# Kernel tuning notes

Measured on AMD Instinct MI355X. Metric: run time of the kernel, lower is better.

The kernel has to match this reference:

```python
import jax, jax.numpy as jnp
import numpy as np

N = 100000
E = 1600000
IN_DIM = 128
HID = 128
OUT_DIM = 64
ORDER = 4


def setup_inputs() -> dict:
    key = jax.random.key(0)
    ks = jax.random.split(key, 10)
    x = jax.random.normal(ks[0], (N, IN_DIM), dtype=jnp.float32)
    edge_index = jax.random.randint(ks[1], (2, E), 0, N, dtype=jnp.int64)
    gen_edge_index = jax.random.randint(ks[2], (2, E), 0, N, dtype=jnp.int64)
    s = 1.0 / np.sqrt(IN_DIM)
    w_orig = jax.random.normal(ks[3], (ORDER + 1, IN_DIM, HID), dtype=jnp.float32) * s
    b_orig = jax.random.normal(ks[4], (ORDER + 1, HID), dtype=jnp.float32) * s
    w_aug = jax.random.normal(ks[5], (ORDER + 1, IN_DIM, HID), dtype=jnp.float32) * s
    b_aug = jax.random.normal(ks[6], (ORDER + 1, HID), dtype=jnp.float32) * s
    fusion_weight = jnp.ones((2,), dtype=jnp.float32)
    clf_w = jax.random.normal(ks[7], (HID, OUT_DIM), dtype=jnp.float32) / np.sqrt(HID)
    clf_b = jax.random.normal(ks[8], (OUT_DIM,), dtype=jnp.float32) / np.sqrt(HID)
    return {"x": x, "edge_index": edge_index, "gen_edge_index": gen_edge_index,
            "w_orig": w_orig, "b_orig": b_orig, "w_aug": w_aug, "b_aug": b_aug,
            "fusion_weight": fusion_weight, "clf_w": clf_w, "clf_b": clf_b}


def _beta_wavelet(x, edge_index, W, b, num_nodes):
    # add self loops
    loop = jnp.arange(num_nodes, dtype=edge_index.dtype)
    row = jnp.concatenate([edge_index[0], loop])
    col = jnp.concatenate([edge_index[1], loop])
    # symmetric normalization D^{-1/2} A D^{-1/2}
    deg = jax.ops.segment_sum(jnp.ones_like(col, dtype=x.dtype), col, num_segments=num_nodes)
    dinv = jnp.where(deg > 0, deg ** -0.5, 0.0)
    norm = dinv[row] * dinv[col]  # [E+N]
    out = x @ W[0] + b[0]
    Tx = x
    for i in range(1, ORDER + 1):
        msg = norm[:, None] * Tx[row]                      # gather + scale [E+N, D]
        Tx = jax.ops.segment_sum(msg, col, num_segments=num_nodes)  # scatter_add
        out = out + Tx @ W[i] + b[i]
    return jax.nn.relu(out)


def reference(x, edge_index, gen_edge_index, w_orig, b_orig, w_aug, b_aug, fusion_weight, clf_w, clf_b):
    num_nodes = x.shape[0]
    h_orig = _beta_wavelet(x, edge_index, w_orig, b_orig, num_nodes)
    h_aug = _beta_wavelet(x, gen_edge_index, w_aug, b_aug, num_nodes)
    w = jax.nn.softmax(fusion_weight)
    h_final = w[0] * h_orig + w[1] * h_aug
    return h_final @ clf_w + clf_b
```

## Files before the change

kernel.cpp:

```cpp
#include <hip/hip_runtime.h>

#define N_NODES 100000
#define NPAD    100096
#define NE      1600000
#define DIM     128
#define ODIM    64
#define NORDER  4
#define KTOT    640
#define NB      391

typedef _Float16 h8 __attribute__((ext_vector_type(8)));
typedef float f4 __attribute__((ext_vector_type(4)));

__device__ __forceinline__ float2 up2(unsigned p) {
    union { unsigned u; _Float16 h[2]; } c; c.u = p;
    return make_float2((float)c.h[0], (float)c.h[1]);
}
__device__ __forceinline__ unsigned pk2(float x, float y) {
    union { unsigned u; _Float16 h[2]; } c;
    c.h[0] = (_Float16)x; c.h[1] = (_Float16)y;
    return c.u;
}
__device__ __forceinline__ unsigned short f2hbits(float x) {
    union { _Float16 h; unsigned short s; } c;
    c.h = (_Float16)x;
    return c.s;
}
__device__ __forceinline__ void async_cp16(const void* g, void* l) {
    __builtin_amdgcn_global_load_lds((const __attribute__((address_space(1))) void*)g,
                                     (__attribute__((address_space(3))) void*)l, 16, 0, 0);
}

__global__ __launch_bounds__(256) void zero_b(int* __restrict__ bhist) {
    int i = blockIdx.x * 256 + threadIdx.x;
    if (i < NB) bhist[i] = 0;
}

__global__ __launch_bounds__(256) void hist_edges(const int* __restrict__ colp,
                                                  int* __restrict__ bhist) {
    __shared__ int lh[NB];
    int t = threadIdx.x;
    for (int i = t; i < NB; i += 256) lh[i] = 0;
    __syncthreads();
    int base = blockIdx.x * 2048 + t;
#pragma unroll
    for (int j = 0; j < 8; ++j) {
        int e = base + j * 256;
        if (e < NE) atomicAdd(&lh[colp[e] >> 8], 1);
    }
    __syncthreads();
    for (int i = t; i < NB; i += 256) if (lh[i]) atomicAdd(&bhist[i], lh[i]);
}

__global__ void bscan(const int* __restrict__ bhist,
                      int* __restrict__ boff,
                      int* __restrict__ bcursor) {
    if (threadIdx.x == 0 && blockIdx.x == 0) {
        int run = 0;
        for (int i = 0; i < NB; ++i) {
            boff[i] = run; bcursor[i] = run; run += bhist[i];
        }
        boff[NB] = run;
    }
}

__global__ __launch_bounds__(256) void part_edges(const int* __restrict__ rowp,
                                                  const int* __restrict__ colp,
                                                  int* __restrict__ bcursor,
                                                  int2* __restrict__ pairs) {
    __shared__ int lh[NB];
    __shared__ int lpos[NB];
    int t = threadIdx.x;
    for (int i = t; i < NB; i += 256) lh[i] = 0;
    __syncthreads();
    int base = blockIdx.x * 4096 + t;
    int rank[16];
    short bk[16];
#pragma unroll
    for (int j = 0; j < 16; ++j) {
        int e = base + j * 256;
        rank[j] = -1;
        if (e < NE) {
            int b = colp[e] >> 8;
            bk[j] = (short)b;
            rank[j] = atomicAdd(&lh[b], 1);
        }
    }
    __syncthreads();
    for (int i = t; i < NB; i += 256) {
        int n = lh[i];
        lpos[i] = n ? atomicAdd(&bcursor[i], n) : 0;
    }
    __syncthreads();
#pragma unroll
    for (int j = 0; j < 16; ++j) {
        int e = base + j * 256;
        if (e < NE) {
            int b = bk[j];
            pairs[lpos[b] + rank[j]] = make_int2(rowp[e], colp[e]);
        }
    }
}

__global__ __launch_bounds__(256) void count_fine(const int2* __restrict__ pairs,
                                                  const int* __restrict__ boff,
                                                  int* __restrict__ cnt) {
    __shared__ int lcnt[256];
    int t = threadIdx.x, b = blockIdx.x;
    lcnt[t] = 0;
    __syncthreads();
    int s = boff[b], e = boff[b + 1];
    int base = b << 8;
    for (int i = s + t; i < e; i += 256)
        atomicAdd(&lcnt[pairs[i].y - base], 1);
    __syncthreads();
    int node = base + t;
    if (node < N_NODES) cnt[node] = lcnt[t];
}

__global__ __launch_bounds__(256) void scan_block(const int* __restrict__ cnt,
                                                  int* __restrict__ excl,
                                                  int* __restrict__ bsum) {
    __shared__ int lds[256];
    int t = threadIdx.x, b = blockIdx.x;
    int base = b * 1024 + t * 4;
    int v0 = (base + 0 < N_NODES) ? cnt[base + 0] : 0;
    int v1 = (base + 1 < N_NODES) ? cnt[base + 1] : 0;
    int v2 = (base + 2 < N_NODES) ? cnt[base + 2] : 0;
    int v3 = (base + 3 < N_NODES) ? cnt[base + 3] : 0;
    int tot = v0 + v1 + v2 + v3;
    lds[t] = tot;
    __syncthreads();
    for (int off = 1; off < 256; off <<= 1) {
        int x = (t >= off) ? lds[t - off] : 0;
        __syncthreads();
        lds[t] += x;
        __syncthreads();
    }
    int run = lds[t] - tot;
    if (t == 255) bsum[b] = lds[255];
    if (base + 0 < N_NODES) excl[base + 0] = run; run += v0;
    if (base + 1 < N_NODES) excl[base + 1] = run; run += v1;
    if (base + 2 < N_NODES) excl[base + 2] = run; run += v2;
    if (base + 3 < N_NODES) excl[base + 3] = run;
}

__global__ void scan_mid(int* __restrict__ bsum, int nb) {
    if (threadIdx.x == 0 && blockIdx.x == 0) {
        int run = 0;
        for (int i = 0; i < nb; ++i) { int x = bsum[i]; bsum[i] = run; run += x; }
    }
}

__global__ __launch_bounds__(256) void scan_add(int* __restrict__ ptrv,
                                                const int* __restrict__ bsum,
                                                const int* __restrict__ cnt,
                                                float* __restrict__ dinv) {
    int i = blockIdx.x * 256 + threadIdx.x;
    if (i < N_NODES) {
        dinv[i] = rsqrtf((float)(cnt[i] + 1));
        ptrv[i] += bsum[i >> 10];
    }
    if (i == 0) ptrv[N_NODES] = NE;
}

__global__ __launch_bounds__(256) void fine_csr(const int2* __restrict__ pairs,
                                                const int* __restrict__ boff,
                                                const int* __restrict__ ptrv,
                                                int* __restrict__ srcv) {
    __shared__ int lcnt[256];
    int t = threadIdx.x, b = blockIdx.x;
    lcnt[t] = 0;
    __syncthreads();
    int s = boff[b], e = boff[b + 1];
    int base = b << 8;
    for (int i = s + t; i < e; i += 256) {
        int2 pr = pairs[i];
        int pos = ptrv[pr.y] + atomicAdd(&lcnt[pr.y - base], 1);
        srcv[pos] = pr.x;
    }
}

__global__ __launch_bounds__(256) void xcast(const float* __restrict__ x,
                                             unsigned* __restrict__ Tbig) {
    int idx = blockIdx.x * 256 + threadIdx.x;
    if (idx >= NPAD * 64) return;
    int m = idx >> 6, u = idx & 63;
    int e = (m << 7) + u * 2;
    float a = (m < N_NODES) ? x[e]     : 0.f;
    float b = (m < N_NODES) ? x[e + 1] : 0.f;
    Tbig[m * 320 + u] = pk2(a, b);
}

__global__ __launch_bounds__(256) void wcast(const float* __restrict__ Wo,
                                             const float* __restrict__ Wa,
                                             unsigned short* __restrict__ Wt) {
    int idx = blockIdx.x * 256 + threadIdx.x;
    if (idx >= 2 * 5 * DIM * DIM) return;
    int g   = idx / (5 * DIM * DIM);
    int rem = idx % (5 * DIM * DIM);
    int i   = rem / (DIM * DIM);
    int r2  = rem % (DIM * DIM);
    int k8  = r2 >> 10;
    int n   = (r2 >> 3) & 127;
    int k7  = r2 & 7;
    int k   = k8 * 8 + k7;
    const float* W = g ? Wa : Wo;
    Wt[idx] = f2hbits(W[(i * DIM + k) * DIM + n]);
}

__global__ __launch_bounds__(256) void propagate(const unsigned* __restrict__ Tin,
                                                 unsigned* __restrict__ Tout,
                                                 const int* __restrict__ ptrv,
                                                 const int* __restrict__ srcv,
                                                 const float* __restrict__ dinv) {
    int gid  = blockIdx.x * 256 + threadIdx.x;
    int lane = threadIdx.x & 63;
    int v    = __builtin_amdgcn_readfirstlane(gid >> 6);
    if (v >= N_NODES) return;
    float dv = dinv[v];
    float2 self = up2(Tin[v * 320 + lane]);
    float ax = dv * dv * self.x;
    float ay = dv * dv * self.y;
    int beg = ptrv[v], end = ptrv[v + 1];
    int k = beg;
    for (; k + 16 <= end; k += 16) {
        int u[16];
#pragma unroll
        for (int j = 0; j < 16; ++j) u[j] = srcv[k + j];
        float2 tt[16];
#pragma unroll
        for (int j = 0; j < 16; ++j) tt[j] = up2(Tin[u[j] * 320 + lane]);
        float w[16];
#pragma unroll
        for (int j = 0; j < 16; ++j) w[j] = dinv[u[j]] * dv;
#pragma unroll
        for (int j = 0; j < 16; ++j) { ax += w[j] * tt[j].x; ay += w[j] * tt[j].y; }
    }
    for (; k + 4 <= end; k += 4) {
        int u[4];
#pragma unroll
        for (int j = 0; j < 4; ++j) u[j] = srcv[k + j];
        float2 tt[4];
#pragma unroll
        for (int j = 0; j < 4; ++j) tt[j] = up2(Tin[u[j] * 320 + lane]);
        float w[4];
#pragma unroll
        for (int j = 0; j < 4; ++j) w[j] = dinv[u[j]] * dv;
#pragma unroll
        for (int j = 0; j < 4; ++j) { ax += w[j] * tt[j].x; ay += w[j] * tt[j].y; }
    }
    for (; k < end; ++k) {
        int u = srcv[k];
        float w = dinv[u] * dv;
        float2 t = up2(Tin[u * 320 + lane]);
        ax += w * t.x; ay += w * t.y;
    }
    Tout[v * 320 + lane] = pk2(ax, ay);
}

__global__ __launch_bounds__(256, 3) void gemmK(const unsigned short* __restrict__ A,
                                                const unsigned short* __restrict__ Wt,
                                                float* __restrict__ C) {
    __shared__ unsigned short Bl[DIM * DIM];
    int t = threadIdx.x;
    int lane = t & 63, wv = t >> 6;
    int m0 = blockIdx.x * 128 + wv * 32;
    int l15 = lane & 15, q = lane >> 4;
    f4 acc[2][8];
#pragma unroll
    for (int mt = 0; mt < 2; ++mt)
#pragma unroll
        for (int nt = 0; nt < 8; ++nt) acc[mt][nt] = (f4)(0.f);

#pragma unroll
    for (int i = 0; i < 5; ++i) {
        const unsigned short* WtI = Wt + (size_t)i * DIM * DIM;
        h8 af[2][4];
#pragma unroll
        for (int mt = 0; mt < 2; ++mt)
#pragma unroll
            for (int kc = 0; kc < 4; ++kc)
                af[mt][kc] = *(const h8*)(A + (size_t)(m0 + mt * 16 + l15) * KTOT
                                            + i * DIM + (kc * 4 + q) * 8);
#pragma unroll
        for (int c = 0; c < 8; ++c) {
            int ci = c * 4 + wv;
            async_cp16(WtI + ci * 512 + lane * 8, &Bl[ci * 512]);
        }
        __syncthreads();
#pragma unroll
        for (int kc = 0; kc < 4; ++kc) {
            int c = kc * 4 + q;
#pragma unroll
            for (int nt = 0; nt < 8; ++nt) {
                h8 bf = *(const h8*)&Bl[(size_t)(c * 128 + nt * 16 + l15) * 8];
                acc[0][nt] = __builtin_amdgcn_mfma_f32_16x16x32_f16(af[0][kc], bf, acc[0][nt], 0, 0, 0);
                acc[1][nt] = __builtin_amdgcn_mfma_f32_16x16x32_f16(af[1][kc], bf, acc[1][nt], 0, 0, 0);
            }
        }
        __syncthreads();
    }
#pragma unroll
    for (int mt = 0; mt < 2; ++mt)
#pragma unroll
        for (int nt = 0; nt < 8; ++nt)
#pragma unroll
            for (int r = 0; r < 4; ++r)
                C[(size_t)(m0 + mt * 16 + q * 4 + r) * DIM + nt * 16 + l15] = acc[mt][nt][r];
}

__global__ __launch_bounds__(256) void fuse_clf(const float* __restrict__ accO,
                                                const float* __restrict__ accA,
                                                const float* __restrict__ bO,
                                                const float* __restrict__ bA,
                                                const float* __restrict__ fw,
                                                const float* __restrict__ clfW,
                                                const float* __restrict__ clfB,
                                                float* __restrict__ out) {
    __shared__ float Wl[DIM * ODIM];
    __shared__ float Hl[32 * DIM];
    __shared__ float bs[2][DIM];
    int t = threadIdx.x;
    float f0 = fw[0], f1 = fw[1];
    float m = fmaxf(f0, f1);
    float e0 = expf(f0 - m), e1 = expf(f1 - m);
    float sw0 = e0 / (e0 + e1), sw1 = e1 / (e0 + e1);
    if (t < 128) {
        float s = 0.f;
        for (int i = 0; i <= NORDER; ++i) s += bO[i * DIM + t];
        bs[0][t] = s;
    } else {
        int j = t - 128;
        float s = 0.f;
        for (int i = 0; i <= NORDER; ++i) s += bA[i * DIM + j];
        bs[1][j] = s;
    }
    for (int i = 0; i < 8; ++i) {
        int idx = (i * 256 + t) * 4;
        *(float4*)&Wl[idx] = *(const float4*)&clfW[idx];
    }
    __syncthreads();
    int rowBase = blockIdx.x * 32;
    for (int i = 0; i < 4; ++i) {
        int idx = (i * 256 + t) * 4;
        int kcol = idx & 127;
        float4 a = *(const float4*)&accO[rowBase * DIM + idx];
        float4 b = *(const float4*)&accA[rowBase * DIM + idx];
        float4 h;
        h.x = sw0 * fmaxf(a.x + bs[0][kcol + 0], 0.f) + sw1 * fmaxf(b.x + bs[1][kcol + 0], 0.f);
        h.y = sw0 * fmaxf(a.y + bs[0][kcol + 1], 0.f) + sw1 * fmaxf(b.y + bs[1][kcol + 1], 0.f);
        h.z = sw0 * fmaxf(a.z + bs[0][kcol + 2], 0.f) + sw1 * fmaxf(b.z + bs[1][kcol + 2], 0.f);
        h.w = sw0 * fmaxf(a.w + bs[0][kcol + 3], 0.f) + sw1 * fmaxf(b.w + bs[1][kcol + 3], 0.f);
        *(float4*)&Hl[idx] = h;
    }
    __syncthreads();
    int lane = t & 63, w = t >> 6;
    int c2 = (lane & 31) * 2;
    int r0 = w * 8 + (lane >> 5) * 4;
    float acc[4][2];
    for (int j = 0; j < 4; ++j) { acc[j][0] = 0.f; acc[j][1] = 0.f; }
    for (int k0 = 0; k0 < DIM; k0 += 4) {
        float4 a0 = *(const float4*)&Hl[(r0 + 0) * DIM + k0];
        float4 a1 = *(const float4*)&Hl[(r0 + 1) * DIM + k0];
        float4 a2 = *(const float4*)&Hl[(r0 + 2) * DIM + k0];
        float4 a3 = *(const float4*)&Hl[(r0 + 3) * DIM + k0];
#define FSTEP(comp, kk)                                                      \
        {                                                                    \
            float2 wv = *(const float2*)&Wl[(k0 + kk) * ODIM + c2];          \
            acc[0][0] += a0.comp * wv.x; acc[0][1] += a0.comp * wv.y;        \
            acc[1][0] += a1.comp * wv.x; acc[1][1] += a1.comp * wv.y;        \
            acc[2][0] += a2.comp * wv.x; acc[2][1] += a2.comp * wv.y;        \
            acc[3][0] += a3.comp * wv.x; acc[3][1] += a3.comp * wv.y;        \
        }
        FSTEP(x, 0) FSTEP(y, 1) FSTEP(z, 2) FSTEP(w, 3)
#undef FSTEP
    }
    float2 cb2 = *(const float2*)&clfB[c2];
    for (int j = 0; j < 4; ++j) {
        float2 o = make_float2(acc[j][0] + cb2.x, acc[j][1] + cb2.y);
        *(float2*)&out[(rowBase + r0 + j) * ODIM + c2] = o;
    }
}

extern "C" void kernel_launch(void* const* d_in, const int* in_sizes, int n_in,
                              void* d_out, int out_size, void* d_ws, size_t ws_size,
                              hipStream_t stream) {
    const float* x   = (const float*)d_in[0];
    const int*   ei  = (const int*)d_in[1];
    const int*   gi  = (const int*)d_in[2];
    const float* w_o = (const float*)d_in[3];
    const float* b_o = (const float*)d_in[4];
    const float* w_a = (const float*)d_in[5];
    const float* b_a = (const float*)d_in[6];
    const float* fw  = (const float*)d_in[7];
    const float* cw  = (const float*)d_in[8];
    const float* cb  = (const float*)d_in[9];
    float* out = (float*)d_out;

    char* p = (char*)d_ws;
    auto alloc = [&](size_t bytes) {
        void* r = (void*)p;
        p += (bytes + 255) & ~(size_t)255;
        return r;
    };
    unsigned* Tbig = (unsigned*)alloc((size_t)NPAD * 320 * 4);
    float* acc_o = (float*)alloc((size_t)NPAD * DIM * 4);
    float* acc_a = (float*)alloc((size_t)NPAD * DIM * 4);
    unsigned short* Wt = (unsigned short*)alloc((size_t)2 * 5 * DIM * DIM * 2);
    float* dinv  = (float*)alloc((size_t)N_NODES * 4);
    int2* pairs  = (int2*)alloc((size_t)NE * 8);
    int* csr_src = (int*)alloc((size_t)NE * 4);
    int* csr_ptr = (int*)alloc((size_t)(N_NODES + 1) * 4);
    int* cnt     = (int*)alloc((size_t)N_NODES * 4);
    int* bsum    = (int*)alloc(128 * 4);
    int* bhist   = (int*)alloc((size_t)NB * 4);
    int* boff    = (int*)alloc((size_t)(NB + 1) * 4);
    int* bcursor = (int*)alloc((size_t)NB * 4);

    const int gN  = (N_NODES + 255) / 256;
    const int gH2 = (NE + 2047) / 2048;
    const int gH4 = (NE + 4095) / 4096;
    const int gS  = (N_NODES + 1023) / 1024;
    const int gP  = (N_NODES * 64 + 255) / 256;
    const int gX  = (NPAD * 64 + 255) / 256;
    const int gW  = (2 * 5 * DIM * DIM + 255) / 256;
    const int gM  = NPAD / 128;
    const int gF  = N_NODES / 32;

    xcast<<<gX, 256, 0, stream>>>(x, Tbig);
    wcast<<<gW, 256, 0, stream>>>(w_o, w_a, Wt);

    for (int g = 0; g < 2; ++g) {
        const int* edges = g ? gi : ei;
        const int* rowp = edges;
        const int* colp = edges + NE;
        float* acc = g ? acc_a : acc_o;
        const unsigned short* Wtg = Wt + (size_t)g * 5 * DIM * DIM;

        zero_b<<<2, 256, 0, stream>>>(bhist);
        hist_edges<<<gH2, 256, 0, stream>>>(colp, bhist);
        bscan<<<1, 64, 0, stream>>>(bhist, boff, bcursor);
        part_edges<<<gH4, 256, 0, stream>>>(rowp, colp, bcursor, pairs);
        count_fine<<<NB, 256, 0, stream>>>(pairs, boff, cnt);
        scan_block<<<gS, 256, 0, stream>>>(cnt, csr_ptr, bsum);
        scan_mid<<<1, 64, 0, stream>>>(bsum, gS);
        scan_add<<<gN, 256, 0, stream>>>(csr_ptr, bsum, cnt, dinv);
        fine_csr<<<NB, 256, 0, stream>>>(pairs, boff, csr_ptr, csr_src);

        for (int i = 1; i <= NORDER; ++i)
            propagate<<<gP, 256, 0, stream>>>(Tbig + (i - 1) * 64, Tbig + i * 64,
                                              csr_ptr, csr_src, dinv);

        gemmK<<<gM, 256, 0, stream>>>((const unsigned short*)Tbig, Wtg, acc);
    }
    fuse_clf<<<gF, 256, 0, stream>>>(acc_o, acc_a, b_o, b_a, fw, cw, cb, out);
}
```

Before: 937.3 us.

## Batch CSR construction for both graphs and pack edge pairs into 32-bit words

```diff
diff --git a/kernel.cpp b/kernel.cpp
--- a/kernel.cpp
+++ b/kernel.cpp
@@ -31,65 +31,91 @@
                                      (__attribute__((address_space(3))) void*)l, 16, 0, 0);
 }
 
-__global__ __launch_bounds__(256) void zero_b(int* __restrict__ bhist) {
-    int i = blockIdx.x * 256 + threadIdx.x;
-    if (i < NB) bhist[i] = 0;
-}
-
-__global__ __launch_bounds__(256) void hist_edges(const int* __restrict__ colp,
+
+__global__ __launch_bounds__(256) void hist_edges(const int* __restrict__ e0,
+                                                  const int* __restrict__ e1,
                                                   int* __restrict__ bhist) {
     __shared__ int lh[NB];
     int t = threadIdx.x;
+    int g = blockIdx.x >= 782;
+    int blk = g ? (blockIdx.x - 782) : blockIdx.x;
+    const int* colp = (g ? e1 : e0) + NE;
+    int* bh = bhist + g * NB;
     for (int i = t; i < NB; i += 256) lh[i] = 0;
     __syncthreads();
-    int base = blockIdx.x * 2048 + t;
+    int base = blk * 2048 + t;
 #pragma unroll
     for (int j = 0; j < 8; ++j) {
         int e = base + j * 256;
         if (e < NE) atomicAdd(&lh[colp[e] >> 8], 1);
     }
     __syncthreads();
-    for (int i = t; i < NB; i += 256) if (lh[i]) atomicAdd(&bhist[i], lh[i]);
-}
-
-__global__ void bscan(const int* __restrict__ bhist,
-                      int* __restrict__ boff,
-                      int* __restrict__ bcursor) {
-    if (threadIdx.x == 0 && blockIdx.x == 0) {
-        int run = 0;
-        for (int i = 0; i < NB; ++i) {
-            boff[i] = run; bcursor[i] = run; run += bhist[i];
-        }
-        boff[NB] = run;
-    }
-}
-
-__global__ __launch_bounds__(256) void part_edges(const int* __restrict__ rowp,
-                                                  const int* __restrict__ colp,
+    for (int i = t; i < NB; i += 256) if (lh[i]) atomicAdd(&bh[i], lh[i]);
+}
+
+__global__ void wave_scan(const int* __restrict__ in,
+                          int* __restrict__ oexcl,
+                          int* __restrict__ ocur,
+                          int n, int with_cur) {
+    int wv = threadIdx.x >> 6, lane = threadIdx.x & 63;
+    if (wv >= 2) return;
+    const int* I = in + wv * n;
+    int* O = oexcl + wv * (n + 1);
+    int* C = ocur + wv * n;
+    int carry = 0;
+    for (int base = 0; base < n; base += 64) {
+        int i = base + lane;
+        int v = (i < n) ? I[i] : 0;
+        int s = v;
+#pragma unroll
+        for (int off = 1; off < 64; off <<= 1) {
+            int x = __shfl_up(s, off, 64);
+            if (lane >= off) s += x;
+        }
+        int excl = carry + s - v;
+        if (i < n) {
+            O[i] = excl;
+            if (with_cur) C[i] = excl;
+        }
+        carry += __shfl(s, 63, 64);
+    }
+    if (lane == 0) O[n] = carry;
+}
+
+__global__ __launch_bounds__(256) void part_edges(const int* __restrict__ e0,
+                                                  const int* __restrict__ e1,
                                                   int* __restrict__ bcursor,
-                                                  int2* __restrict__ pairs) {
+                                                  unsigned* __restrict__ pairs) {
     __shared__ int lh[NB];
     __shared__ int lpos[NB];
     int t = threadIdx.x;
+    int g = blockIdx.x >= NB;
+    int blk = g ? (blockIdx.x - NB) : blockIdx.x;
+    const int* rowp = (g ? e1 : e0);
+    const int* colp = rowp + NE;
+    int* bc = bcursor + g * NB;
+    unsigned* pr = pairs + (size_t)g * NE;
     for (int i = t; i < NB; i += 256) lh[i] = 0;
     __syncthreads();
-    int base = blockIdx.x * 4096 + t;
+    int base = blk * 4096 + t;
     int rank[16];
     short bk[16];
+    unsigned char lcv[16];
 #pragma unroll
     for (int j = 0; j < 16; ++j) {
         int e = base + j * 256;
         rank[j] = -1;
         if (e < NE) {
-            int b = colp[e] >> 8;
-            bk[j] = (short)b;
-            rank[j] = atomicAdd(&lh[b], 1);
+            int c = colp[e];
+            bk[j] = (short)(c >> 8);
+            lcv[j] = (unsigned char)(c & 255);
+            rank[j] = atomicAdd(&lh[c >> 8], 1);
         }
     }
     __syncthreads();
     for (int i = t; i < NB; i += 256) {
         int n = lh[i];
-        lpos[i] = n ? atomicAdd(&bcursor[i], n) : 0;
+        lpos[i] = n ? atomicAdd(&bc[i], n) : 0;
     }
     __syncthreads();
 #pragma unroll
@@ -97,87 +123,82 @@
         int e = base + j * 256;
         if (e < NE) {
             int b = bk[j];
-            pairs[lpos[b] + rank[j]] = make_int2(rowp[e], colp[e]);
-        }
-    }
-}
-
-__global__ __launch_bounds__(256) void count_fine(const int2* __restrict__ pairs,
-                                                  const int* __restrict__ boff,
-                                                  int* __restrict__ cnt) {
+            pr[lpos[b] + rank[j]] = ((unsigned)rowp[e] << 8) | lcv[j];
+        }
+    }
+}
+
+__global__ __launch_bounds__(256) void cnt_scan(const unsigned* __restrict__ pairs,
+                                                const int* __restrict__ boff,
+                                                int* __restrict__ ptrv,
+                                                float* __restrict__ dinv,
+                                                int* __restrict__ bsum) {
     __shared__ int lcnt[256];
-    int t = threadIdx.x, b = blockIdx.x;
+    __shared__ int lscan[256];
+    int t = threadIdx.x;
+    int g = blockIdx.x >= NB;
+    int b = g ? (blockIdx.x - NB) : blockIdx.x;
+    const unsigned* pr = pairs + (size_t)g * NE;
+    const int* bo = boff + g * (NB + 1);
+    int* pv = ptrv + g * (N_NODES + 1);
+    float* dv = dinv + g * N_NODES;
+    int* bs = bsum + g * NB;
     lcnt[t] = 0;
     __syncthreads();
-    int s = boff[b], e = boff[b + 1];
-    int base = b << 8;
+    int s = bo[b], e = bo[b + 1];
     for (int i = s + t; i < e; i += 256)
-        atomicAdd(&lcnt[pairs[i].y - base], 1);
-    __syncthreads();
-    int node = base + t;
-    if (node < N_NODES) cnt[node] = lcnt[t];
-}
-
-__global__ __launch_bounds__(256) void scan_block(const int* __restrict__ cnt,
-                                                  int* __restrict__ excl,
-                                                  int* __restrict__ bsum) {
-    __shared__ int lds[256];
-    int t = threadIdx.x, b = blockIdx.x;
-    int base = b * 1024 + t * 4;
-    int v0 = (base + 0 < N_NODES) ? cnt[base + 0] : 0;
-    int v1 = (base + 1 < N_NODES) ? cnt[base + 1] : 0;
-    int v2 = (base + 2 < N_NODES) ? cnt[base + 2] : 0;
-    int v3 = (base + 3 < N_NODES) ? cnt[base + 3] : 0;
-    int tot = v0 + v1 + v2 + v3;
-    lds[t] = tot;
+        atomicAdd(&lcnt[pr[i] & 255u], 1);
+    __syncthreads();
+    int v = lcnt[t];
+    lscan[t] = v;
     __syncthreads();
     for (int off = 1; off < 256; off <<= 1) {
-        int x = (t >= off) ? lds[t - off] : 0;
+        int x = (t >= off) ? lscan[t - off] : 0;
         __syncthreads();
-        lds[t] += x;
+        lscan[t] += x;
         __syncthreads();
     }
-    int run = lds[t] - tot;
-    if (t == 255) bsum[b] = lds[255];
-    if (base + 0 < N_NODES) excl[base + 0] = run; run += v0;
-    if (base + 1 < N_NODES) excl[base + 1] = run; run += v1;
-    if (base + 2 < N_NODES) excl[base + 2] = run; run += v2;
-    if (base + 3 < N_NODES) excl[base + 3] = run;
-}
-
-__global__ void scan_mid(int* __restrict__ bsum, int nb) {
-    if (threadIdx.x == 0 && blockIdx.x == 0) {
-        int run = 0;
-        for (int i = 0; i < nb; ++i) { int x = bsum[i]; bsum[i] = run; run += x; }
-    }
-}
-
-__global__ __launch_bounds__(256) void scan_add(int* __restrict__ ptrv,
-                                                const int* __restrict__ bsum,
-                                                const int* __restrict__ cnt,
-                                                float* __restrict__ dinv) {
-    int i = blockIdx.x * 256 + threadIdx.x;
-    if (i < N_NODES) {
-        dinv[i] = rsqrtf((float)(cnt[i] + 1));
-        ptrv[i] += bsum[i >> 10];
-    }
-    if (i == 0) ptrv[N_NODES] = NE;
-}
-
-__global__ __launch_bounds__(256) void fine_csr(const int2* __restrict__ pairs,
+    int node = (b << 8) + t;
+    if (node < N_NODES) {
+        pv[node] = lscan[t] - v;
+        dv[node] = rsqrtf((float)(v + 1));
+    }
+    if (t == 255) bs[b] = lscan[255];
+}
+
+__global__ __launch_bounds__(256) void scan_addk(int* __restrict__ ptrv,
+                                                 const int* __restrict__ bmid) {
+    int t = threadIdx.x;
+    int g = blockIdx.x >= NB;
+    int b = g ? (blockIdx.x - NB) : blockIdx.x;
+    int* pv = ptrv + g * (N_NODES + 1);
+    const int* bm = bmid + g * (NB + 1);
+    int node = (b << 8) + t;
+    if (node < N_NODES) pv[node] += bm[b];
+    if (b == 0 && t == 0) pv[N_NODES] = NE;
+}
+
+__global__ __launch_bounds__(256) void fine_csr(const unsigned* __restrict__ pairs,
                                                 const int* __restrict__ boff,
                                                 const int* __restrict__ ptrv,
                                                 int* __restrict__ srcv) {
     __shared__ int lcnt[256];
-    int t = threadIdx.x, b = blockIdx.x;
+    int t = threadIdx.x;
+    int g = blockIdx.x >= NB;
+    int b = g ? (blockIdx.x - NB) : blockIdx.x;
+    const unsigned* pr = pairs + (size_t)g * NE;
+    const int* bo = boff + g * (NB + 1);
+    const int* pv = ptrv + g * (N_NODES + 1);
+    int* sv = srcv + (size_t)g * NE;
     lcnt[t] = 0;
     __syncthreads();
-    int s = boff[b], e = boff[b + 1];
+    int s = bo[b], e = bo[b + 1];
     int base = b << 8;
     for (int i = s + t; i < e; i += 256) {
-        int2 pr = pairs[i];
-        int pos = ptrv[pr.y] + atomicAdd(&lcnt[pr.y - base], 1);
-        srcv[pos] = pr.x;
+        unsigned pk = pr[i];
+        int lc = (int)(pk & 255u);
+        int pos = pv[base + lc] + atomicAdd(&lcnt[lc], 1);
+        sv[pos] = (int)(pk >> 8);
     }
 }
 
@@ -408,20 +429,16 @@
     float* acc_o = (float*)alloc((size_t)NPAD * DIM * 4);
     float* acc_a = (float*)alloc((size_t)NPAD * DIM * 4);
     unsigned short* Wt = (unsigned short*)alloc((size_t)2 * 5 * DIM * DIM * 2);
-    float* dinv  = (float*)alloc((size_t)N_NODES * 4);
-    int2* pairs  = (int2*)alloc((size_t)NE * 8);
-    int* csr_src = (int*)alloc((size_t)NE * 4);
-    int* csr_ptr = (int*)alloc((size_t)(N_NODES + 1) * 4);
-    int* cnt     = (int*)alloc((size_t)N_NODES * 4);
-    int* bsum    = (int*)alloc(128 * 4);
-    int* bhist   = (int*)alloc((size_t)NB * 4);
-    int* boff    = (int*)alloc((size_t)(NB + 1) * 4);
-    int* bcursor = (int*)alloc((size_t)NB * 4);
-
-    const int gN  = (N_NODES + 255) / 256;
-    const int gH2 = (NE + 2047) / 2048;
-    const int gH4 = (NE + 4095) / 4096;
-    const int gS  = (N_NODES + 1023) / 1024;
+    float* dinv  = (float*)alloc((size_t)2 * N_NODES * 4);
+    unsigned* pairs = (unsigned*)alloc((size_t)2 * NE * 4);
+    int* csr_src = (int*)alloc((size_t)2 * NE * 4);
+    int* csr_ptr = (int*)alloc((size_t)2 * (N_NODES + 1) * 4);
+    int* bhist   = (int*)alloc((size_t)2 * NB * 4);
+    int* boff    = (int*)alloc((size_t)2 * (NB + 1) * 4);
+    int* bcursor = (int*)alloc((size_t)2 * NB * 4);
+    int* bsum    = (int*)alloc((size_t)2 * NB * 4);
+    int* bmid    = (int*)alloc((size_t)2 * (NB + 1) * 4);
+
     const int gP  = (N_NODES * 64 + 255) / 256;
     const int gX  = (NPAD * 64 + 255) / 256;
     const int gW  = (2 * 5 * DIM * DIM + 255) / 256;
@@ -431,26 +448,25 @@
     xcast<<<gX, 256, 0, stream>>>(x, Tbig);
     wcast<<<gW, 256, 0, stream>>>(w_o, w_a, Wt);
 
+    hipMemsetAsync(bhist, 0, (size_t)2 * NB * 4, stream);
+    hist_edges<<<2 * 782, 256, 0, stream>>>(ei, gi, bhist);
+    wave_scan<<<1, 128, 0, stream>>>(bhist, boff, bcursor, NB, 1);
+    part_edges<<<2 * NB, 256, 0, stream>>>(ei, gi, bcursor, pairs);
+    cnt_scan<<<2 * NB, 256, 0, stream>>>(pairs, boff, csr_ptr, dinv, bsum);
+    wave_scan<<<1, 128, 0, stream>>>(bsum, bmid, bcursor, NB, 0);
+    scan_addk<<<2 * NB, 256, 0, stream>>>(csr_ptr, bmid);
+    fine_csr<<<2 * NB, 256, 0, stream>>>(pairs, boff, csr_ptr, csr_src);
+
     for (int g = 0; g < 2; ++g) {
-        const int* edges = g ? gi : ei;
-        const int* rowp = edges;
-        const int* colp = edges + NE;
         float* acc = g ? acc_a : acc_o;
         const unsigned short* Wtg = Wt + (size_t)g * 5 * DIM * DIM;
-
-        zero_b<<<2, 256, 0, stream>>>(bhist);
-        hist_edges<<<gH2, 256, 0, stream>>>(colp, bhist);
-        bscan<<<1, 64, 0, stream>>>(bhist, boff, bcursor);
-        part_edges<<<gH4, 256, 0, stream>>>(rowp, colp, bcursor, pairs);
-        count_fine<<<NB, 256, 0, stream>>>(pairs, boff, cnt);
-        scan_block<<<gS, 256, 0, stream>>>(cnt, csr_ptr, bsum);
-        scan_mid<<<1, 64, 0, stream>>>(bsum, gS);
-        scan_add<<<gN, 256, 0, stream>>>(csr_ptr, bsum, cnt, dinv);
-        fine_csr<<<NB, 256, 0, stream>>>(pairs, boff, csr_ptr, csr_src);
+        const int* pv = csr_ptr + g * (N_NODES + 1);
+        const int* sv = csr_src + (size_t)g * NE;
+        const float* dv = dinv + (size_t)g * N_NODES;
 
         for (int i = 1; i <= NORDER; ++i)
             propagate<<<gP, 256, 0, stream>>>(Tbig + (i - 1) * 64, Tbig + i * 64,
-                                              csr_ptr, csr_src, dinv);
+                                              pv, sv, dv);
 
         gemmK<<<gM, 256, 0, stream>>>((const unsigned short*)Tbig, Wtg, acc);
     }
```

After: 864.6 us. 7.8% less time.
